# Kernel optimization log

Hardware: AMD Instinct MI355X
Metric: run time of the kernel (lower is better)

Reference implementation:

```python
import jax, jax.numpy as jnp
import numpy as np

N_NODES = 50000
N_EDGES = 800000
IN_CH = 128
HID = 128
OUT_CH = 16
N_LAYERS = 3
N_GRAPHS = 128
BN_EPS = 1e-5


def setup_inputs() -> dict:
    key = jax.random.key(0)
    ks = jax.random.split(key, 12)
    x = jax.random.normal(ks[0], (N_NODES, IN_CH), dtype=jnp.float32)
    edge_index = jax.random.randint(ks[1], (2, N_EDGES), 0, N_NODES, dtype=jnp.int64)
    batch = jnp.sort(jax.random.randint(ks[2], (N_NODES,), 0, N_GRAPHS, dtype=jnp.int64))
    s = 1.0 / np.sqrt(HID)
    W1 = jax.random.normal(ks[3], (N_LAYERS, IN_CH, HID), dtype=jnp.float32) * s
    b1 = jax.random.normal(ks[4], (N_LAYERS, HID), dtype=jnp.float32) * s
    W2 = jax.random.normal(ks[5], (N_LAYERS, HID, HID), dtype=jnp.float32) * s
    b2 = jax.random.normal(ks[6], (N_LAYERS, HID), dtype=jnp.float32) * s
    gamma = jnp.ones((N_LAYERS, HID), dtype=jnp.float32)
    beta = jnp.zeros((N_LAYERS, HID), dtype=jnp.float32)
    mean = jax.random.normal(ks[7], (N_LAYERS, HID), dtype=jnp.float32) * 0.1
    var = jax.random.uniform(ks[8], (N_LAYERS, HID), dtype=jnp.float32, minval=0.5, maxval=1.5)
    Wc = jax.random.normal(ks[9], (HID, OUT_CH), dtype=jnp.float32) * s
    bc = jax.random.normal(ks[10], (OUT_CH,), dtype=jnp.float32) * s
    return {"x": x, "edge_index": edge_index, "batch": batch, "W1": W1, "b1": b1,
            "W2": W2, "b2": b2, "gamma": gamma, "beta": beta, "mean": mean,
            "var": var, "Wc": Wc, "bc": bc}


def reference(x, edge_index, batch, W1, b1, W2, b2, gamma, beta, mean, var, Wc, bc):
    # GIN (eval mode: BN uses running stats, dropout is identity).
    src, dst = edge_index[0], edge_index[1]
    n = x.shape[0]
    h = x
    for i in range(N_LAYERS):
        # GINConv with eps=0: MLP(x + sum_{j->i} x_j)
        agg = jax.ops.segment_sum(h[src], dst, num_segments=n)  # [N, d]
        z = h + agg
        z = jnp.maximum(z @ W1[i] + b1[i], 0.0) @ W2[i] + b2[i]  # 2-layer MLP
        # BatchNorm1d (eval) + ReLU
        inv = gamma[i] * jax.lax.rsqrt(var[i] + BN_EPS)
        h = jnp.maximum((z - mean[i]) * inv + beta[i], 0.0)
    pooled = jax.ops.segment_sum(h, batch, num_segments=N_GRAPHS)  # [G, hid]
    return pooled @ Wc + bc
```

## Files before the change

### kernel.cpp

```cpp
#include <hip/hip_runtime.h>

#define N_NODES 50000
#define N_EDGES 800000
#define CH 128
#define N_GRAPHS 128
#define N_LAYERS 3
#define OUT_CH 16
#define BN_EPS 1e-5f
#define NSPLIT 16
#define NB 196
#define BCAP 4608
#define EPB 4096
#define NTILES (N_NODES / 16)
#define SSTRIDE 20
#define CB 6250
#define SB 196
#define PB 388

typedef unsigned short ushort_t;
typedef __attribute__((ext_vector_type(8))) short bf16x8;
typedef __attribute__((ext_vector_type(4))) float f32x4;

__device__ inline ushort_t f2b(float f) {
    unsigned u = __float_as_uint(f);
    unsigned r = (u + 0x7fffu + ((u >> 16) & 1u)) >> 16;
    return (ushort_t)r;
}
__device__ inline float b2f(ushort_t b) { return __uint_as_float((unsigned)b << 16); }
__device__ inline float blo(unsigned u) { return __uint_as_float(u << 16); }
__device__ inline float bhi(unsigned u) { return __uint_as_float(u & 0xffff0000u); }

__global__ __launch_bounds__(256) void setup_kernel(
    const float4* __restrict__ x, ushort4* __restrict__ xb, int* __restrict__ gcur,
    const int* __restrict__ batch, int* __restrict__ starts, float* __restrict__ pooled,
    const float* __restrict__ W1, const float* __restrict__ W2, ushort_t* __restrict__ Wt,
    const float* __restrict__ b1, const float* __restrict__ b2,
    const float* __restrict__ gamma, const float* __restrict__ beta,
    const float* __restrict__ mean, const float* __restrict__ var,
    float* __restrict__ scale, float* __restrict__ shift) {
    int bid = blockIdx.x, t = threadIdx.x;
    if (bid < CB) {
        int i = bid * 256 + t;
        if (i < NB) gcur[i] = 0;
        float4 v = x[i];
        ushort4 o;
        o.x = f2b(v.x); o.y = f2b(v.y); o.z = f2b(v.z); o.w = f2b(v.w);
        xb[i] = o;
    } else if (bid < CB + SB) {
        int i = (bid - CB) * 256 + t;
        if (i < N_GRAPHS * CH) pooled[i] = 0.f;
        if (i >= N_NODES) return;
        int b = batch[i];
        if (i == 0) {
            for (int g = 0; g <= b; ++g) starts[g] = 0;
        } else {
            int pb = batch[i - 1];
            for (int g = pb + 1; g <= b; ++g) starts[g] = i;
        }
        if (i == N_NODES - 1) {
            for (int g = b + 1; g <= N_GRAPHS; ++g) starts[g] = N_NODES;
        }
    } else {
        int i = (bid - CB - SB) * 256 + t;
        if (i < 6 * CH * CH) {
            int mat = i >> 14, r = i & 16383;
            int j = r & 7, bb = r >> 3;
            int lane = bb & 63, cs = bb >> 6;
            int ct = cs >> 2, ks = cs & 3;
            int n = ct * 16 + (lane & 15);
            int k = ks * 32 + (lane >> 4) * 8 + j;
            const float* Wsrc = (mat < 3) ? (W1 + (size_t)mat * CH * CH)
                                          : (W2 + (size_t)(mat - 3) * CH * CH);
            Wt[i] = f2b(Wsrc[k * CH + n]);
        } else {
            int e = i - 6 * CH * CH;
            if (e >= 6 * CH) return;
            int mat = e / CH, c = e % CH;
            if (mat < 3) {
                scale[e] = 1.f;
                shift[e] = b1[mat * CH + c];
            } else {
                int l = mat - 3;
                float inv = gamma[l * CH + c] * rsqrtf(var[l * CH + c] + BN_EPS);
                scale[e] = inv;
                shift[e] = (b2[l * CH + c] - mean[l * CH + c]) * inv + beta[l * CH + c];
            }
        }
    }
}

__global__ __launch_bounds__(256) void bin_kernel(const int* __restrict__ src,
                                                  const int* __restrict__ dst,
                                                  int* __restrict__ gcur,
                                                  unsigned* __restrict__ gbuck) {
    __shared__ int lcnt[256];
    __shared__ int lpref[256];
    __shared__ int lpos[NB];
    __shared__ int lbase[NB];
    __shared__ unsigned stage[EPB];
    __shared__ unsigned char sbk[EPB];
    int t = threadIdx.x;
    int e0 = blockIdx.x * EPB;
    int nloc = N_EDGES - e0; if (nloc > EPB) nloc = EPB;

    lcnt[t] = 0;
    __syncthreads();

    int2 ed[16];
    #pragma unroll
    for (int j = 0; j < 16; ++j) {
        int i = j * 256 + t;
        if (i < nloc) {
            ed[j].x = src[e0 + i];
            ed[j].y = dst[e0 + i];
            atomicAdd(&lcnt[ed[j].y >> 8], 1);
        } else ed[j].y = -1;
    }
    __syncthreads();
    int v = lcnt[t];
    lpref[t] = v;
    __syncthreads();
    for (int off = 1; off < 256; off <<= 1) {
        int y = (t >= off) ? lpref[t - off] : 0;
        __syncthreads();
        lpref[t] += y;
        __syncthreads();
    }
    int excl = lpref[t] - v;
    __syncthreads();
    lpref[t] = excl;
    if (t < NB) {
        lpos[t] = excl;
        lbase[t] = atomicAdd(&gcur[t], v);
    }
    __syncthreads();
    #pragma unroll
    for (int j = 0; j < 16; ++j) {
        if (ed[j].y >= 0) {
            int b = ed[j].y >> 8;
            int slot = atomicAdd(&lpos[b], 1);
            stage[slot] = (unsigned)ed[j].x | ((unsigned)(ed[j].y & 255) << 16);
            sbk[slot] = (unsigned char)b;
        }
    }
    __syncthreads();
    for (int i = t; i < nloc; i += 256) {
        int b = sbk[i];
        gbuck[(size_t)b * BCAP + lbase[b] + (i - lpref[b])] = stage[i];
    }
}

__global__ __launch_bounds__(256) void place_kernel(const int* __restrict__ gcur,
                                                    const unsigned* __restrict__ gbuck,
                                                    int* __restrict__ rowptr,
                                                    ushort_t* __restrict__ esrc) {
    __shared__ ushort_t ssrc[BCAP];
    __shared__ unsigned char sd[BCAP];
    __shared__ int outS[BCAP];
    __shared__ int cnt[256], pref[256], cur[256];
    __shared__ int sscan[256];
    int b = blockIdx.x, t = threadIdx.x;
    int gv = (t < NB) ? gcur[t] : 0;
    sscan[t] = gv;
    cnt[t] = 0;
    __syncthreads();
    for (int off = 1; off < 256; off <<= 1) {
        int y = (t >= off) ? sscan[t - off] : 0;
        __syncthreads();
        sscan[t] += y;
        __syncthreads();
    }
    int nb = gcur[b];
    int base = sscan[b] - nb;
    for (int i = t; i < nb; i += 256) {
        unsigned p = gbuck[(size_t)b * BCAP + i];
        ssrc[i] = (ushort_t)(p & 0xffffu);
        int dl = (p >> 16) & 0xff;
        sd[i] = (unsigned char)dl;
        atomicAdd(&cnt[dl], 1);
    }
    __syncthreads();
    int v = cnt[t];
    pref[t] = v;
    __syncthreads();
    for (int off = 1; off < 256; off <<= 1) {
        int y = (t >= off) ? pref[t - off] : 0;
        __syncthreads();
        pref[t] += y;
        __syncthreads();
    }
    int excl = pref[t] - v;
    __syncthreads();
    pref[t] = excl;
    cur[t] = 0;
    int idx = (b << 8) + t;
    if (idx < N_NODES) rowptr[idx] = base + excl;
    if (b == NB - 1 && t == 0) rowptr[N_NODES] = N_EDGES;
    __syncthreads();
    for (int i = t; i < nb; i += 256) {
        int dl = sd[i];
        int p = pref[dl] + atomicAdd(&cur[dl], 1);
        outS[p] = ssrc[i];
    }
    __syncthreads();
    for (int i = t; i < nb; i += 256)
        esrc[base + i] = (ushort_t)outS[i];
}

__global__ __launch_bounds__(256) void agg_kernel(const unsigned* __restrict__ h2,
                                                  const int* __restrict__ rowptr,
                                                  const ushort_t* __restrict__ esrc,
                                                  unsigned* __restrict__ z2) {
    int wid = (blockIdx.x * 256 + threadIdx.x) >> 6;
    int lane = threadIdx.x & 63;
    if (wid >= N_NODES) return;
    unsigned self = h2[(size_t)wid * 64 + lane];
    float ax = blo(self), ay = bhi(self);
    int e = rowptr[wid], end = rowptr[wid + 1];
    for (; e + 16 <= end; e += 16) {
        unsigned u[16];
        #pragma unroll
        for (int j = 0; j < 16; ++j) {
            int s = esrc[e + j];
            u[j] = h2[(size_t)s * 64 + lane];
        }
        #pragma unroll
        for (int j = 0; j < 16; ++j) { ax += blo(u[j]); ay += bhi(u[j]); }
    }
    for (; e + 8 <= end; e += 8) {
        unsigned u[8];
        #pragma unroll
        for (int j = 0; j < 8; ++j) {
            int s = esrc[e + j];
            u[j] = h2[(size_t)s * 64 + lane];
        }
        #pragma unroll
        for (int j = 0; j < 8; ++j) { ax += blo(u[j]); ay += bhi(u[j]); }
    }
    for (; e + 4 <= end; e += 4) {
        unsigned u[4];
        #pragma unroll
        for (int j = 0; j < 4; ++j) {
            int s = esrc[e + j];
            u[j] = h2[(size_t)s * 64 + lane];
        }
        #pragma unroll
        for (int j = 0; j < 4; ++j) { ax += blo(u[j]); ay += bhi(u[j]); }
    }
    for (; e < end; ++e) {
        unsigned u = h2[(size_t)esrc[e] * 64 + lane];
        ax += blo(u); ay += bhi(u);
    }
    z2[(size_t)wid * 64 + lane] = ((unsigned)f2b(ay) << 16) | (unsigned)f2b(ax);
}

__global__ __launch_bounds__(512) void mlp_kernel(const ushort_t* __restrict__ A,
                                                  const ushort_t* __restrict__ Wf1,
                                                  const ushort_t* __restrict__ Wf2,
                                                  const float* __restrict__ shift1,
                                                  const float* __restrict__ scale2,
                                                  const float* __restrict__ shift2,
                                                  ushort_t* __restrict__ Out) {
    __shared__ ushort_t sW1[CH * CH];
    __shared__ ushort_t sW2[CH * CH];
    __shared__ ushort_t sS[8][CH * SSTRIDE];

    int t = threadIdx.x;
    int wave = t >> 6, lane = t & 63;
    int quad = lane >> 4, l16 = lane & 15;

    {
        const uint4* g1 = (const uint4*)Wf1;
        const uint4* g2 = (const uint4*)Wf2;
        uint4* s1 = (uint4*)sW1;
        uint4* s2 = (uint4*)sW2;
        for (int i = t; i < 2048; i += 512) { s1[i] = g1[i]; s2[i] = g2[i]; }
    }
    __syncthreads();

    const bf16x8* w1f = (const bf16x8*)sW1;
    const bf16x8* w2f = (const bf16x8*)sW2;
    int wg = blockIdx.x * 8 + wave;

    for (int it = 0; it < 2; ++it) {
        int tile = wg + 2048 * it;
        if (tile >= NTILES) break;
        int arow = tile * 16 + l16;

        bf16x8 af[4];
        #pragma unroll
        for (int ks = 0; ks < 4; ++ks)
            af[ks] = *(const bf16x8*)(A + (size_t)arow * CH + ks * 32 + quad * 8);

        f32x4 acc[8];
        #pragma unroll
        for (int ct = 0; ct < 8; ++ct) acc[ct] = (f32x4){0.f, 0.f, 0.f, 0.f};
        #pragma unroll
        for (int ct = 0; ct < 8; ++ct)
            #pragma unroll
            for (int ks = 0; ks < 4; ++ks)
                acc[ct] = __builtin_amdgcn_mfma_f32_16x16x32_bf16(
                    af[ks], w1f[(ct * 4 + ks) * 64 + lane], acc[ct], 0, 0, 0);

        #pragma unroll
        for (int ct = 0; ct < 8; ++ct) {
            int k = ct * 16 + l16;
            float sh = shift1[k];
            uint2 p;
            p.x = ((unsigned)f2b(fmaxf(acc[ct][1] + sh, 0.f)) << 16)
                |  (unsigned)f2b(fmaxf(acc[ct][0] + sh, 0.f));
            p.y = ((unsigned)f2b(fmaxf(acc[ct][3] + sh, 0.f)) << 16)
                |  (unsigned)f2b(fmaxf(acc[ct][2] + sh, 0.f));
            *(uint2*)&sS[wave][k * SSTRIDE + quad * 4] = p;
        }

        bf16x8 af2[4];
        #pragma unroll
        for (int ks = 0; ks < 4; ++ks)
            #pragma unroll
            for (int j = 0; j < 8; ++j)
                af2[ks][j] = (short)sS[wave][(ks * 32 + quad * 8 + j) * SSTRIDE + l16];

        f32x4 acc2[8];
        #pragma unroll
        for (int ct = 0; ct < 8; ++ct) acc2[ct] = (f32x4){0.f, 0.f, 0.f, 0.f};
        #pragma unroll
        for (int ct = 0; ct < 8; ++ct)
            #pragma unroll
            for (int ks = 0; ks < 4; ++ks)
                acc2[ct] = __builtin_amdgcn_mfma_f32_16x16x32_bf16(
                    af2[ks], w2f[(ct * 4 + ks) * 64 + lane], acc2[ct], 0, 0, 0);

        int row0 = tile * 16;
        #pragma unroll
        for (int ct = 0; ct < 8; ++ct) {
            int col = ct * 16 + l16;
            float sc = scale2[col], sh = shift2[col];
            #pragma unroll
            for (int r = 0; r < 4; ++r) {
                int row = row0 + quad * 4 + r;
                Out[(size_t)row * CH + col] = f2b(fmaxf(acc2[ct][r] * sc + sh, 0.f));
            }
        }
    }
}

__global__ __launch_bounds__(64) void pool_kernel(const unsigned* __restrict__ h2,
                                                  const int* __restrict__ starts,
                                                  float* __restrict__ pooled) {
    int g = blockIdx.x >> 4, s = blockIdx.x & 15;
    int c = threadIdx.x;
    int beg = starts[g], end = starts[g + 1];
    float s0 = 0.f, s1 = 0.f;
    for (int n = beg + s; n < end; n += NSPLIT) {
        unsigned u = h2[(size_t)n * 64 + c];
        s0 += blo(u); s1 += bhi(u);
    }
    atomicAdd(&pooled[g * CH + 2 * c], s0);
    atomicAdd(&pooled[g * CH + 2 * c + 1], s1);
}

__global__ __launch_bounds__(256) void cls_kernel(const float* __restrict__ pooled,
                                                  const float* __restrict__ Wc,
                                                  const float* __restrict__ bc,
                                                  float* __restrict__ out) {
    int i = blockIdx.x * blockDim.x + threadIdx.x;
    if (i >= N_GRAPHS * OUT_CH) return;
    int g = i / OUT_CH, o = i % OUT_CH;
    float s = bc[o];
    for (int k = 0; k < CH; ++k) s += pooled[g * CH + k] * Wc[k * OUT_CH + o];
    out[i] = s;
}

extern "C" void kernel_launch(void* const* d_in, const int* in_sizes, int n_in,
                              void* d_out, int out_size, void* d_ws, size_t ws_size,
                              hipStream_t stream) {
    const float* x     = (const float*)d_in[0];
    const int*   eidx  = (const int*)d_in[1];
    const int*   batch = (const int*)d_in[2];
    const float* W1    = (const float*)d_in[3];
    const float* b1    = (const float*)d_in[4];
    const float* W2    = (const float*)d_in[5];
    const float* b2    = (const float*)d_in[6];
    const float* gamma = (const float*)d_in[7];
    const float* beta  = (const float*)d_in[8];
    const float* mean  = (const float*)d_in[9];
    const float* var   = (const float*)d_in[10];
    const float* Wc    = (const float*)d_in[11];
    const float* bc    = (const float*)d_in[12];
    float* out = (float*)d_out;

    const int* src = eidx;
    const int* dst = eidx + N_EDGES;

    char* w = (char*)d_ws;
    size_t off = 0;
    auto alloc = [&](size_t bytes) { void* p = w + off; off += (bytes + 255) & ~(size_t)255; return p; };
    int*      gcur   = (int*)alloc(NB * 4);
    unsigned* gbuck  = (unsigned*)alloc((size_t)NB * BCAP * 4);
    int*      rowptr = (int*)alloc((N_NODES + 1) * 4);
    ushort_t* esrc   = (ushort_t*)alloc(N_EDGES * 2);
    int*      starts = (int*)alloc((N_GRAPHS + 1) * 4);
    ushort_t* Bh     = (ushort_t*)alloc((size_t)N_NODES * CH * 2);
    ushort_t* Bz     = (ushort_t*)alloc((size_t)N_NODES * CH * 2);
    ushort_t* Wt     = (ushort_t*)alloc((size_t)6 * CH * CH * 2);
    float*    scale  = (float*)alloc(6 * CH * 4);
    float*    shift  = (float*)alloc(6 * CH * 4);
    float*    pooled = (float*)alloc(N_GRAPHS * CH * 4);
    (void)ws_size; (void)n_in; (void)in_sizes; (void)out_size;

    setup_kernel<<<CB + SB + PB, 256, 0, stream>>>(
        (const float4*)x, (ushort4*)Bh, gcur,
        batch, starts, pooled,
        W1, W2, Wt, b1, b2, gamma, beta, mean, var, scale, shift);
    bin_kernel<<<(N_EDGES + EPB - 1) / EPB, 256, 0, stream>>>(src, dst, gcur, gbuck);
    place_kernel<<<NB, 256, 0, stream>>>(gcur, gbuck, rowptr, esrc);

    const int agg_grid = (N_NODES + 3) / 4;

    for (int i = 0; i < N_LAYERS; ++i) {
        agg_kernel<<<agg_grid, 256, 0, stream>>>((const unsigned*)Bh, rowptr, esrc,
                                                 (unsigned*)Bz);
        mlp_kernel<<<256, 512, 0, stream>>>(Bz,
                                            Wt + (size_t)i * CH * CH,
                                            Wt + (size_t)(3 + i) * CH * CH,
                                            shift + i * CH,
                                            scale + (3 + i) * CH,
                                            shift + (3 + i) * CH,
                                            Bh);
    }

    pool_kernel<<<N_GRAPHS * NSPLIT, 64, 0, stream>>>((const unsigned*)Bh, starts, pooled);
    cls_kernel<<<(N_GRAPHS * OUT_CH + 255) / 256, 256, 0, stream>>>(pooled, Wc, bc, out);
}
```

Measured before the change: 271.2 us.

## Split node features into four channel-quarter planes and aggregate per quarter

```diff
diff --git a/kernel.cpp b/kernel.cpp
--- a/kernel.cpp
+++ b/kernel.cpp
@@ -13,6 +13,8 @@
 #define EPB 4096
 #define NTILES (N_NODES / 16)
 #define SSTRIDE 20
+#define QS  ((size_t)N_NODES * 16)
+#define QS2 ((size_t)N_NODES * 32)
 #define CB 6250
 #define SB 196
 #define PB 388
@@ -31,7 +33,7 @@
 __device__ inline float bhi(unsigned u) { return __uint_as_float(u & 0xffff0000u); }
 
 __global__ __launch_bounds__(256) void setup_kernel(
-    const float4* __restrict__ x, ushort4* __restrict__ xb, int* __restrict__ gcur,
+    const float4* __restrict__ x, ushort_t* __restrict__ xb, int* __restrict__ gcur,
     const int* __restrict__ batch, int* __restrict__ starts, float* __restrict__ pooled,
     const float* __restrict__ W1, const float* __restrict__ W2, ushort_t* __restrict__ Wt,
     const float* __restrict__ b1, const float* __restrict__ b2,
@@ -42,10 +44,12 @@
     if (bid < CB) {
         int i = bid * 256 + t;
         if (i < NB) gcur[i] = 0;
+        int node = i >> 5, v4 = i & 31;
+        int q = v4 >> 3, co = (v4 & 7) * 4;
         float4 v = x[i];
         ushort4 o;
         o.x = f2b(v.x); o.y = f2b(v.y); o.z = f2b(v.z); o.w = f2b(v.w);
-        xb[i] = o;
+        *(ushort4*)&xb[(size_t)q * QS2 + (size_t)node * 32 + co] = o;
     } else if (bid < CB + SB) {
         int i = (bid - CB) * 256 + t;
         if (i < N_GRAPHS * CH) pooled[i] = 0.f;
@@ -207,51 +211,45 @@
         esrc[base + i] = (ushort_t)outS[i];
 }
 
-__global__ __launch_bounds__(256) void agg_kernel(const unsigned* __restrict__ h2,
-                                                  const int* __restrict__ rowptr,
-                                                  const ushort_t* __restrict__ esrc,
-                                                  unsigned* __restrict__ z2) {
+__global__ __launch_bounds__(256) void aggq_kernel(const unsigned* __restrict__ hq,
+                                                   const int* __restrict__ rowptr,
+                                                   const ushort_t* __restrict__ esrc,
+                                                   unsigned* __restrict__ zq) {
     int wid = (blockIdx.x * 256 + threadIdx.x) >> 6;
     int lane = threadIdx.x & 63;
     if (wid >= N_NODES) return;
-    unsigned self = h2[(size_t)wid * 64 + lane];
-    float ax = blo(self), ay = bhi(self);
+    int slot = lane >> 4, ld = lane & 15;
+    float ax = 0.f, ay = 0.f;
     int e = rowptr[wid], end = rowptr[wid + 1];
     for (; e + 16 <= end; e += 16) {
-        unsigned u[16];
-        #pragma unroll
-        for (int j = 0; j < 16; ++j) {
-            int s = esrc[e + j];
-            u[j] = h2[(size_t)s * 64 + lane];
-        }
-        #pragma unroll
-        for (int j = 0; j < 16; ++j) { ax += blo(u[j]); ay += bhi(u[j]); }
-    }
-    for (; e + 8 <= end; e += 8) {
-        unsigned u[8];
-        #pragma unroll
-        for (int j = 0; j < 8; ++j) {
-            int s = esrc[e + j];
-            u[j] = h2[(size_t)s * 64 + lane];
-        }
-        #pragma unroll
-        for (int j = 0; j < 8; ++j) { ax += blo(u[j]); ay += bhi(u[j]); }
+        unsigned u[4];
+        #pragma unroll
+        for (int it = 0; it < 4; ++it) {
+            int s = __builtin_nontemporal_load(&esrc[e + it * 4 + slot]);
+            u[it] = hq[(unsigned)s * 16 + ld];
+        }
+        #pragma unroll
+        for (int it = 0; it < 4; ++it) { ax += blo(u[it]); ay += bhi(u[it]); }
     }
     for (; e + 4 <= end; e += 4) {
-        unsigned u[4];
-        #pragma unroll
-        for (int j = 0; j < 4; ++j) {
-            int s = esrc[e + j];
-            u[j] = h2[(size_t)s * 64 + lane];
-        }
-        #pragma unroll
-        for (int j = 0; j < 4; ++j) { ax += blo(u[j]); ay += bhi(u[j]); }
-    }
-    for (; e < end; ++e) {
-        unsigned u = h2[(size_t)esrc[e] * 64 + lane];
+        int s = __builtin_nontemporal_load(&esrc[e + slot]);
+        unsigned u = hq[(unsigned)s * 16 + ld];
         ax += blo(u); ay += bhi(u);
     }
-    z2[(size_t)wid * 64 + lane] = ((unsigned)f2b(ay) << 16) | (unsigned)f2b(ax);
+    if (e < end) {
+        int m = end - e;
+        int s = __builtin_nontemporal_load(&esrc[(slot < m) ? e + slot : e]);
+        unsigned u = hq[(unsigned)s * 16 + ld];
+        if (slot < m) { ax += blo(u); ay += bhi(u); }
+    }
+    ax += __shfl_xor(ax, 16); ax += __shfl_xor(ax, 32);
+    ay += __shfl_xor(ay, 16); ay += __shfl_xor(ay, 32);
+    if (lane < 16) {
+        unsigned self = hq[(unsigned)wid * 16 + lane];
+        float fx = ax + blo(self), fy = ay + bhi(self);
+        unsigned pk = ((unsigned)f2b(fy) << 16) | (unsigned)f2b(fx);
+        __builtin_nontemporal_store(pk, &zq[(unsigned)wid * 16 + lane]);
+    }
 }
 
 __global__ __launch_bounds__(512) void mlp_kernel(const ushort_t* __restrict__ A,
@@ -290,7 +288,7 @@
         bf16x8 af[4];
         #pragma unroll
         for (int ks = 0; ks < 4; ++ks)
-            af[ks] = *(const bf16x8*)(A + (size_t)arow * CH + ks * 32 + quad * 8);
+            af[ks] = *(const bf16x8*)(A + (size_t)ks * QS2 + (size_t)arow * 32 + quad * 8);
 
         f32x4 acc[8];
         #pragma unroll
@@ -336,10 +334,12 @@
         for (int ct = 0; ct < 8; ++ct) {
             int col = ct * 16 + l16;
             float sc = scale2[col], sh = shift2[col];
+            int qc = col >> 5, co = col & 31;
             #pragma unroll
             for (int r = 0; r < 4; ++r) {
                 int row = row0 + quad * 4 + r;
-                Out[(size_t)row * CH + col] = f2b(fmaxf(acc2[ct][r] * sc + sh, 0.f));
+                Out[(size_t)qc * QS2 + (size_t)row * 32 + co] =
+                    f2b(fmaxf(acc2[ct][r] * sc + sh, 0.f));
             }
         }
     }
@@ -350,14 +350,17 @@
                                                   float* __restrict__ pooled) {
     int g = blockIdx.x >> 4, s = blockIdx.x & 15;
     int c = threadIdx.x;
+    int q = c >> 4, ld = c & 15;
+    const unsigned* hq = h2 + (size_t)q * QS;
     int beg = starts[g], end = starts[g + 1];
     float s0 = 0.f, s1 = 0.f;
     for (int n = beg + s; n < end; n += NSPLIT) {
-        unsigned u = h2[(size_t)n * 64 + c];
+        unsigned u = hq[(size_t)n * 16 + ld];
         s0 += blo(u); s1 += bhi(u);
     }
-    atomicAdd(&pooled[g * CH + 2 * c], s0);
-    atomicAdd(&pooled[g * CH + 2 * c + 1], s1);
+    int ch = q * 32 + 2 * ld;
+    atomicAdd(&pooled[g * CH + ch], s0);
+    atomicAdd(&pooled[g * CH + ch + 1], s1);
 }
 
 __global__ __launch_bounds__(256) void cls_kernel(const float* __restrict__ pooled,
@@ -410,24 +413,29 @@
     (void)ws_size; (void)n_in; (void)in_sizes; (void)out_size;
 
     setup_kernel<<<CB + SB + PB, 256, 0, stream>>>(
-        (const float4*)x, (ushort4*)Bh, gcur,
+        (const float4*)x, Bh, gcur,
         batch, starts, pooled,
         W1, W2, Wt, b1, b2, gamma, beta, mean, var, scale, shift);
     bin_kernel<<<(N_EDGES + EPB - 1) / EPB, 256, 0, stream>>>(src, dst, gcur, gbuck);
     place_kernel<<<NB, 256, 0, stream>>>(gcur, gbuck, rowptr, esrc);
 
-    const int agg_grid = (N_NODES + 3) / 4;
-
+    const int aggq_grid = (N_NODES + 3) / 4;
+
+    ushort_t* hbuf = Bh;
+    ushort_t* zbuf = Bz;
     for (int i = 0; i < N_LAYERS; ++i) {
-        agg_kernel<<<agg_grid, 256, 0, stream>>>((const unsigned*)Bh, rowptr, esrc,
-                                                 (unsigned*)Bz);
-        mlp_kernel<<<256, 512, 0, stream>>>(Bz,
+        for (int q = 0; q < 4; ++q) {
+            aggq_kernel<<<aggq_grid, 256, 0, stream>>>(
+                (const unsigned*)(hbuf + (size_t)q * QS2), rowptr, esrc,
+                (unsigned*)(zbuf + (size_t)q * QS2));
+        }
+        mlp_kernel<<<256, 512, 0, stream>>>(zbuf,
                                             Wt + (size_t)i * CH * CH,
                                             Wt + (size_t)(3 + i) * CH * CH,
                                             shift + i * CH,
                                             scale + (3 + i) * CH,
                                             shift + (3 + i) * CH,
-                                            Bh);
+                                            hbuf);
     }
 
     pool_kernel<<<N_GRAPHS * NSPLIT, 64, 0, stream>>>((const unsigned*)Bh, starts, pooled);
```

New measurement: 468.7 us. +72.8%, slower.
